# Kernel optimization log

Hardware: AMD Instinct MI355X
Metric: run time of the kernel (lower is better)

## Reference

```python
import jax, jax.numpy as jnp
import numpy as np

NG, NPG = 16384, 8            # graphs, nodes per graph
N = NG * NPG                   # total nodes
EPS = 1e-5                     # BatchNorm eps
SLOPE = 0.01                   # leaky_relu negative slope
DIMS = [6, 16, 16, 32, 64, 128]


def _gcn(x, src, dst, w_e, W, b):
    # PyG GCNConv with edge weights and implicit self-loops (weight 1):
    # h = x W; out = D^-1/2 (A + I) D^-1/2 h + b, deg from dst incl. self-loop
    h = x @ W
    deg = jnp.zeros((N,), h.dtype).at[dst].add(w_e) + 1.0
    dis = jax.lax.rsqrt(deg)
    norm = dis[src] * w_e * dis[dst]                      # [E]
    out = jnp.zeros_like(h).at[dst].add(norm[:, None] * h[src])
    out = out + h * (dis * dis)[:, None]                  # self-loop term deg^-1 * h
    return out + b


def _bn(x, g, be):
    # training-mode BatchNorm1d over nodes (biased variance)
    m = x.mean(0)
    v = ((x - m) ** 2).mean(0)
    return g * (x - m) * jax.lax.rsqrt(v + EPS) + be


def _lrelu(x):
    return jnp.where(x >= 0, x, SLOPE * x)


def setup_inputs() -> dict:
    key = jax.random.key(0)
    ks = jax.random.split(key, 16)
    # fully-connected directed edges within each 8-node graph (no self-loops)
    s, d = np.meshgrid(np.arange(NPG), np.arange(NPG), indexing='ij')
    m = s != d
    s, d = s[m], d[m]                                     # 56 per graph
    offs = (np.arange(NG) * NPG)[:, None]
    src = (offs + s[None, :]).ravel()
    dst = (offs + d[None, :]).ravel()
    E = src.size
    inp = {
        'x': jax.random.normal(ks[0], (N, DIMS[0]), jnp.float32),
        'edge_index': jnp.asarray(np.stack([src, dst]), dtype=jnp.int32),
        'edge_attr': jax.random.uniform(ks[1], (E,), jnp.float32),
        'batch': jnp.asarray(np.repeat(np.arange(NG), NPG), dtype=jnp.int32),
    }
    for i in range(5):
        inp[f'w{i+1}'] = jax.random.normal(ks[2 + i], (DIMS[i], DIMS[i + 1]), jnp.float32) * (1.0 / np.sqrt(DIMS[i]).astype(np.float32))
        inp[f'b{i+1}'] = jnp.zeros((DIMS[i + 1],), jnp.float32)
        inp[f'g{i+1}'] = jnp.ones((DIMS[i + 1],), jnp.float32)
        inp[f'be{i+1}'] = jnp.zeros((DIMS[i + 1],), jnp.float32)
    inp['fc1_w'] = jax.random.normal(ks[7], (128, 30), jnp.float32) * 0.1
    inp['fc1_b'] = jnp.zeros((30,), jnp.float32)
    inp['fc2_w'] = jax.random.normal(ks[8], (30, 20), jnp.float32) * 0.1
    inp['fc2_b'] = jnp.zeros((20,), jnp.float32)
    inp['out_w'] = jax.random.normal(ks[9], (20, 1), jnp.float32) * 0.1
    inp['out_b'] = jnp.zeros((1,), jnp.float32)
    return inp


def reference(x, edge_index, edge_attr, batch,
              w1, b1, g1, be1, w2, b2, g2, be2, w3, b3, g3, be3,
              w4, b4, g4, be4, w5, b5, g5, be5,
              fc1_w, fc1_b, fc2_w, fc2_b, out_w, out_b):
    src, dst = edge_index[0], edge_index[1]
    layers = [(w1, b1, g1, be1), (w2, b2, g2, be2), (w3, b3, g3, be3),
              (w4, b4, g4, be4), (w5, b5, g5, be5)]
    h = x
    for (W, b, g, be) in layers:
        h = _lrelu(_bn(_gcn(h, src, dst, edge_attr, W, b), g, be))
    # global mean pool: each graph has exactly NPG nodes
    pooled = jax.ops.segment_sum(h, batch, num_segments=NG) / NPG
    z = _lrelu(pooled @ fc1_w + fc1_b)
    z = _lrelu(z @ fc2_w + fc2_b)      # dropout is identity in eval mode
    return z @ out_w + out_b           # [NG, 1]
```

## Files before the change

kernel.cpp:

```cpp
#include <hip/hip_runtime.h>

#define NN 131072
#define NBLK 256
#define THREADS 512
#define NODES_B 512
#define GRAPHS_B 64
constexpr float BN_EPS = 1e-5f;
constexpr float NSLOPE = 0.01f;

typedef unsigned short ushortT;
typedef unsigned long long u64;
typedef short v8s __attribute__((ext_vector_type(8)));
typedef float v4f __attribute__((ext_vector_type(4)));

__device__ __forceinline__ float lrelu(float x) { return x >= 0.0f ? x : NSLOPE * x; }
__device__ __forceinline__ ushortT f2bf(float f) {
    unsigned int u = __float_as_uint(f);
    u += 0x7fffu + ((u >> 16) & 1u);
    return (ushortT)(u >> 16);
}

__device__ __forceinline__ u64 enc_stat(float t) {
    long long v = (long long)llrintf(t * 65536.0f) + (1LL << 41);
    return (1ULL << 52) + (u64)v;
}
__device__ __forceinline__ float dec_stat(u64 u) {
    long long v = (long long)(u & ((1ULL << 52) - 1)) - ((long long)NBLK << 41);
    return (float)((double)v * (1.0 / 65536.0));
}

__global__ void zero_ws_kernel(u64* __restrict__ p) {
    for (int i = threadIdx.x; i < 4096; i += 1024) p[i] = 0ULL;
}

struct Params {
    const float *x, *ea;
    const float *w1,*b1,*g1,*be1, *w2,*b2,*g2,*be2, *w3,*b3,*g3,*be3;
    const float *w4,*b4,*g4,*be4, *w5,*b5,*g5,*be5;
    const float *fc1w,*fc1b,*fc2w,*fc2b,*ow,*ob;
    u64* stats;
    float* outp;
};

template<int DIN>
__device__ __forceinline__ void agg_shfl(const float* xr, float* Y, const float* coef,
                                         int lane, int d) {
    #pragma unroll
    for (int k = 0; k < DIN; k++) Y[k] = coef[0] * xr[k];
    #pragma unroll
    for (int r = 1; r < 8; r++) {
        int srcLane = (lane & ~7) | ((d + r) & 7);
        float cr = coef[r];
        #pragma unroll
        for (int k = 0; k < DIN; k++)
            Y[k] = fmaf(cr, __shfl(xr[k], srcLane), Y[k]);
    }
}

template<int DIN, int DOUT>
__device__ __forceinline__ void gemm_lane(const float* Y, const float* Wl,
                                          const float* bias, float* acc) {
    #pragma unroll
    for (int j = 0; j < DOUT; j++) acc[j] = bias[j];
    #pragma unroll
    for (int k = 0; k < DIN; k++) {
        float yk = Y[k];
        #pragma unroll
        for (int j = 0; j < DOUT; j++)
            acc[j] = fmaf(yk, Wl[k * DOUT + j], acc[j]);
    }
}

template<int DOUT>
__device__ __forceinline__ void stats_from_hbuf(const float* hbuf, float* red,
                                                u64* statsL, int tid) {
    __syncthreads();
    constexpr int SEG = THREADS / DOUT;
    int c = tid % DOUT, seg = tid / DOUT;
    float s = 0.f, q = 0.f;
    #pragma unroll 4
    for (int i = 0; i < DOUT; i++) {
        float v = hbuf[(seg * DOUT + i) * 33 + c];
        s += v; q = fmaf(v, v, q);
    }
    red[seg * 2 * DOUT + c] = s;
    red[seg * 2 * DOUT + DOUT + c] = q;
    __syncthreads();
    if (tid < 2 * DOUT) {
        float t = 0.f;
        #pragma unroll
        for (int sg = 0; sg < SEG; sg++) t += red[sg * 2 * DOUT + tid];
        __hip_atomic_fetch_add(&statsL[tid * 8], enc_stat(t),
                               __ATOMIC_RELAXED, __HIP_MEMORY_SCOPE_AGENT);
    }
}

template<int DIN>
__device__ __forceinline__ void bn_params(const u64* statsL, const float* g,
                                          const float* be, float* scS, float* shS, int tid) {
    __syncthreads();
    if (tid < DIN) {
        u64 us, uq;
        int guard = 0;
        do {
            us = __hip_atomic_load(&statsL[tid * 8], __ATOMIC_RELAXED, __HIP_MEMORY_SCOPE_AGENT);
        } while ((us >> 52) < (u64)NBLK && ++guard < (1 << 26));
        guard = 0;
        do {
            uq = __hip_atomic_load(&statsL[(DIN + tid) * 8], __ATOMIC_RELAXED, __HIP_MEMORY_SCOPE_AGENT);
        } while ((uq >> 52) < (u64)NBLK && ++guard < (1 << 26));
        float s = dec_stat(us), q = dec_stat(uq);
        float mean = s * (1.0f / NN);
        float var = fmaf(-mean, mean, q * (1.0f / NN));
        float scl = g[tid] * rsqrtf(var + BN_EPS);
        scS[tid] = scl;
        shS[tid] = fmaf(-mean, scl, be[tid]);
    }
    __syncthreads();
}

__device__ __forceinline__ v8s ld_v8(const ushortT* p) {
    union { v8s v; uint2 u[2]; } t;
    t.u[0] = *(const uint2*)p;
    t.u[1] = *(const uint2*)(p + 4);
    return t.v;
}

#define SMEM_TOTAL 153472

__global__ __launch_bounds__(THREADS, 2) void fused_kernel(Params P)
{
    __shared__ __align__(16) char smem[SMEM_TOTAL];
    float*   hbuf   = (float*)smem;
    ushortT* Y4b    = (ushortT*)smem;
    ushortT* X5T    = (ushortT*)smem;
    float*   pooled = (float*)smem;
    float*   WesS   = (float*)(smem + 67584);
    float*   disS   = (float*)(smem + 81920);
    float*   AcS    = (float*)(smem + 83968);
    ushortT* X4T    = (ushortT*)(smem + 67584);
    ushortT* Y5b    = (ushortT*)(smem + 67584);
    float*   z1s    = (float*)(smem + 67584);
    float*   z2s    = (float*)(smem + 75776);
    float*   W123   = (float*)(smem + 137216);
    ushortT* W4t    = (ushortT*)(smem + 140672);
    float*   red    = (float*)(smem + 145280);
    float*   scS    = red;
    float*   shS    = red + 128;

    const int tid  = threadIdx.x;
    const int bid  = blockIdx.x;
    const int lane = tid & 63;
    const int w    = tid >> 6;
    const int m16  = lane & 15;
    const int quad = lane >> 4;
    const int d    = tid & 7;
    const int gloc = tid >> 3;

    const int g0 = bid * GRAPHS_B;
    for (int e = tid; e < GRAPHS_B * 56; e += THREADS) WesS[e] = P.ea[(size_t)g0 * 56 + e];
    if (tid < 96)  W123[tid] = P.w1[tid];
    if (tid < 256) W123[96 + tid] = P.w2[tid];
    W123[352 + tid] = P.w3[tid];
    for (int e = tid; e < 2048; e += THREADS) {
        int c = e >> 5, k = e & 31;
        W4t[c * 36 + k] = f2bf(P.w4[(size_t)k * 64 + c]);
    }
    __syncthreads();

    {
        float deg = 1.0f;
        #pragma unroll
        for (int s = 0; s < 8; s++)
            if (s != d) deg += WesS[gloc * 56 + s * 7 + (d > s ? d - 1 : d)];
        disS[tid] = rsqrtf(deg);
    }
    __syncthreads();

    float coef[8];
    {
        float dis = disS[tid];
        coef[0] = dis * dis;
        #pragma unroll
        for (int r = 1; r < 8; r++) {
            int s = (d + r) & 7;
            float we = WesS[gloc * 56 + s * 7 + (d > s ? d - 1 : d)];
            coef[r] = dis * we * disS[(tid & ~7) | s];
        }
    }
    for (int e = tid; e < GRAPHS_B * 64; e += THREADS) {
        int g = e >> 6, s = (e >> 3) & 7, dd = e & 7;
        float v;
        if (s == dd) { float t = disS[g * 8 + dd]; v = t * t; }
        else v = disS[g * 8 + s] * WesS[g * 56 + s * 7 + (dd > s ? dd - 1 : dd)] * disS[g * 8 + dd];
        AcS[g * 68 + s * 8 + dd] = v;
    }
    __syncthreads();

    v8s AcM[4];
    #pragma unroll
    for (int Gl = 0; Gl < 4; Gl++) {
        int G = 4 * w + Gl;
        int koct = 2 * (G & 1) + (m16 >> 3);
        int gA = 2 * G + (m16 >> 3);
        ushortT tmp[8];
        #pragma unroll
        for (int j = 0; j < 8; j++)
            tmp[j] = (quad == koct) ? f2bf(AcS[gA * 68 + j * 8 + (m16 & 7)]) : (ushortT)0;
        AcM[Gl] = *(v8s*)tmp;
    }
    v8s W5f[8][2];
    #pragma unroll
    for (int ct = 0; ct < 8; ct++)
        #pragma unroll
        for (int kh = 0; kh < 2; kh++) {
            ushortT tmp[8];
            #pragma unroll
            for (int j = 0; j < 8; j++)
                tmp[j] = f2bf(P.w5[(size_t)(kh * 32 + quad * 8 + j) * 128 + ct * 16 + m16]);
            W5f[ct][kh] = *(v8s*)tmp;
        }

    const int gnode = bid * NODES_B + tid;
    float xr[16];
    {
        const float2* px = (const float2*)(P.x + (size_t)gnode * 6);
        float2 a = px[0], b = px[1], c = px[2];
        xr[0]=a.x; xr[1]=a.y; xr[2]=b.x; xr[3]=b.y; xr[4]=c.x; xr[5]=c.y;
    }
    {
        float Y[6], acc[16];
        agg_shfl<6>(xr, Y, coef, lane, d);
        gemm_lane<6,16>(Y, W123, P.b1, acc);
        #pragma unroll
        for (int j = 0; j < 16; j++) hbuf[tid * 33 + j] = acc[j];
    }
    stats_from_hbuf<16>(hbuf, red, P.stats + 0, tid);
    bn_params<16>(P.stats + 0, P.g1, P.be1, scS, shS, tid);

    {
        #pragma unroll
        for (int k = 0; k < 16; k++)
            xr[k] = lrelu(fmaf(scS[k], hbuf[tid * 33 + k], shS[k]));
        float Y[16], acc[16];
        agg_shfl<16>(xr, Y, coef, lane, d);
        gemm_lane<16,16>(Y, W123 + 96, P.b2, acc);
        #pragma unroll
        for (int j = 0; j < 16; j++) hbuf[tid * 33 + j] = acc[j];
    }
    stats_from_hbuf<16>(hbuf, red, P.stats + 32 * 8, tid);
    bn_params<16>(P.stats + 32 * 8, P.g2, P.be2, scS, shS, tid);

    {
        #pragma unroll
        for (int k = 0; k < 16; k++)
            xr[k] = lrelu(fmaf(scS[k], hbuf[tid * 33 + k], shS[k]));
        float Y[16], acc[32];
        agg_shfl<16>(xr, Y, coef, lane, d);
        gemm_lane<16,32>(Y, W123 + 352, P.b3, acc);
        #pragma unroll
        for (int j = 0; j < 32; j++) hbuf[tid * 33 + j] = acc[j];
    }
    stats_from_hbuf<32>(hbuf, red, P.stats + 64 * 8, tid);
    bn_params<32>(P.stats + 64 * 8, P.g3, P.be3, scS, shS, tid);

    #pragma unroll
    for (int it = 0; it < 8; it++) {
        int item = tid + it * THREADS;
        int c = item & 31, nq = item >> 5;
        float sc = scS[c], sh = shS[c];
        ushortT pk[4];
        #pragma unroll
        for (int i = 0; i < 4; i++)
            pk[i] = f2bf(lrelu(fmaf(sc, hbuf[(nq * 4 + i) * 33 + c], sh)));
        *(uint2*)&X4T[c * 520 + nq * 4] = *(uint2*)pk;
    }
    __syncthreads();

    {
        v8s Bf[2][2];
        #pragma unroll
        for (int Jl = 0; Jl < 2; Jl++) {
            int J = 2 * w + Jl;
            #pragma unroll
            for (int ct = 0; ct < 2; ct++)
                Bf[Jl][ct] = ld_v8(&X4T[(ct * 16 + m16) * 520 + 32 * J + quad * 8]);
        }
        #pragma unroll
        for (int Gl = 0; Gl < 4; Gl++) {
            int G = 4 * w + Gl;
            #pragma unroll
            for (int ct = 0; ct < 2; ct++) {
                v4f a = (v4f){0.f, 0.f, 0.f, 0.f};
                a = __builtin_amdgcn_mfma_f32_16x16x32_bf16(AcM[Gl], Bf[Gl >> 1][ct], a, 0, 0, 0);
                int ch = ct * 16 + m16;
                #pragma unroll
                for (int r = 0; r < 4; r++)
                    Y4b[(G * 16 + quad * 4 + r) * 36 + ch] = f2bf(a[r]);
            }
        }
    }
    __syncthreads();

    float b4r[4];
    #pragma unroll
    for (int ct = 0; ct < 4; ct++) b4r[ct] = P.b4[ct * 16 + m16];
    v4f acc4[4][4];
    {
        v8s W4fr[4];
        #pragma unroll
        for (int ct = 0; ct < 4; ct++)
            W4fr[ct] = ld_v8(&W4t[(ct * 16 + m16) * 36 + quad * 8]);
        #pragma unroll
        for (int rt = 0; rt < 4; rt++) {
            v8s Af = ld_v8(&Y4b[(w * 64 + rt * 16 + m16) * 36 + quad * 8]);
            #pragma unroll
            for (int ct = 0; ct < 4; ct++) {
                v4f a = (v4f){0.f, 0.f, 0.f, 0.f};
                a = __builtin_amdgcn_mfma_f32_16x16x32_bf16(Af, W4fr[ct], a, 0, 0, 0);
                #pragma unroll
                for (int r = 0; r < 4; r++) a[r] += b4r[ct];
                acc4[rt][ct] = a;
            }
        }
    }
    {
        float ps[4], pq[4];
        #pragma unroll
        for (int ct = 0; ct < 4; ct++) { ps[ct] = 0.f; pq[ct] = 0.f; }
        #pragma unroll
        for (int rt = 0; rt < 4; rt++)
            #pragma unroll
            for (int ct = 0; ct < 4; ct++)
                #pragma unroll
                for (int r = 0; r < 4; r++) {
                    float v = acc4[rt][ct][r];
                    ps[ct] += v; pq[ct] = fmaf(v, v, pq[ct]);
                }
        __syncthreads();
        #pragma unroll
        for (int ct = 0; ct < 4; ct++) {
            float s = ps[ct], q = pq[ct];
            s += __shfl_xor(s, 16); s += __shfl_xor(s, 32);
            q += __shfl_xor(q, 16); q += __shfl_xor(q, 32);
            if (lane < 16) {
                red[w * 256 + ct * 16 + lane] = s;
                red[w * 256 + 64 + ct * 16 + lane] = q;
            }
        }
        __syncthreads();
        if (tid < 128) {
            float t = 0.f;
            #pragma unroll
            for (int ww = 0; ww < 8; ww++) t += red[ww * 256 + tid];
            __hip_atomic_fetch_add(&P.stats[(128 + tid) * 8], enc_stat(t),
                                   __ATOMIC_RELAXED, __HIP_MEMORY_SCOPE_AGENT);
        }
    }
    bn_params<64>(P.stats + 128 * 8, P.g4, P.be4, scS, shS, tid);

    #pragma unroll
    for (int rt = 0; rt < 4; rt++) {
        int nd0 = w * 64 + rt * 16 + quad * 4;
        #pragma unroll
        for (int ct = 0; ct < 4; ct++) {
            int c = ct * 16 + m16;
            float sc = scS[c], sh = shS[c];
            ushortT pk[4];
            #pragma unroll
            for (int r = 0; r < 4; r++)
                pk[r] = f2bf(lrelu(fmaf(sc, acc4[rt][ct][r], sh)));
            *(uint2*)&X5T[c * 520 + nd0] = *(uint2*)pk;
        }
    }
    __syncthreads();

    {
        v8s Bf[2][4];
        #pragma unroll
        for (int Jl = 0; Jl < 2; Jl++) {
            int J = 2 * w + Jl;
            #pragma unroll
            for (int ct = 0; ct < 4; ct++)
                Bf[Jl][ct] = ld_v8(&X5T[(ct * 16 + m16) * 520 + 32 * J + quad * 8]);
        }
        #pragma unroll
        for (int Gl = 0; Gl < 4; Gl++) {
            int G = 4 * w + Gl;
            #pragma unroll
            for (int ct = 0; ct < 4; ct++) {
                v4f a = (v4f){0.f, 0.f, 0.f, 0.f};
                a = __builtin_amdgcn_mfma_f32_16x16x32_bf16(AcM[Gl], Bf[Gl >> 1][ct], a, 0, 0, 0);
                int ch = ct * 16 + m16;
                #pragma unroll
                for (int r = 0; r < 4; r++)
                    Y5b[(G * 16 + quad * 4 + r) * 68 + ch] = f2bf(a[r]);
            }
        }
    }
    __syncthreads();

    float b5r[8];
    #pragma unroll
    for (int ct = 0; ct < 8; ct++) b5r[ct] = P.b5[ct * 16 + m16];
    v4f acc5[4][8];
    #pragma unroll
    for (int rt = 0; rt < 4; rt++) {
        v8s Af0 = ld_v8(&Y5b[(w * 64 + rt * 16 + m16) * 68 + quad * 8]);
        v8s Af1 = ld_v8(&Y5b[(w * 64 + rt * 16 + m16) * 68 + 32 + quad * 8]);
        #pragma unroll
        for (int ct = 0; ct < 8; ct++) {
            v4f a = (v4f){0.f, 0.f, 0.f, 0.f};
            a = __builtin_amdgcn_mfma_f32_16x16x32_bf16(Af0, W5f[ct][0], a, 0, 0, 0);
            a = __builtin_amdgcn_mfma_f32_16x16x32_bf16(Af1, W5f[ct][1], a, 0, 0, 0);
            #pragma unroll
            for (int r = 0; r < 4; r++) a[r] += b5r[ct];
            acc5[rt][ct] = a;
        }
    }
    {
        float ps[8], pq[8];
        #pragma unroll
        for (int ct = 0; ct < 8; ct++) { ps[ct] = 0.f; pq[ct] = 0.f; }
        #pragma unroll
        for (int rt = 0; rt < 4; rt++)
            #pragma unroll
            for (int ct = 0; ct < 8; ct++)
                #pragma unroll
                for (int r = 0; r < 4; r++) {
                    float v = acc5[rt][ct][r];
                    ps[ct] += v; pq[ct] = fmaf(v, v, pq[ct]);
                }
        __syncthreads();
        #pragma unroll
        for (int ct = 0; ct < 8; ct++) {
            float s = ps[ct], q = pq[ct];
            s += __shfl_xor(s, 16); s += __shfl_xor(s, 32);
            q += __shfl_xor(q, 16); q += __shfl_xor(q, 32);
            if (lane < 16) {
                red[w * 256 + ct * 16 + lane] = s;
                red[w * 256 + 128 + ct * 16 + lane] = q;
            }
        }
        __syncthreads();
        if (tid < 256) {
            float t = 0.f;
            #pragma unroll
            for (int ww = 0; ww < 8; ww++) t += red[ww * 256 + tid];
            __hip_atomic_fetch_add(&P.stats[(256 + tid) * 8], enc_stat(t),
                                   __ATOMIC_RELAXED, __HIP_MEMORY_SCOPE_AGENT);
        }
    }
    bn_params<128>(P.stats + 256 * 8, P.g5, P.be5, scS, shS, tid);

    #pragma unroll
    for (int rt = 0; rt < 4; rt++) {
        int gA = 8 * w + 2 * rt + (quad >> 1);
        #pragma unroll
        for (int ct = 0; ct < 8; ct++) {
            int c = ct * 16 + m16;
            float sc = scS[c], sh = shS[c];
            float p = 0.f;
            #pragma unroll
            for (int r = 0; r < 4; r++)
                p += lrelu(fmaf(sc, acc5[rt][ct][r], sh));
            p += __shfl_xor(p, 16);
            if ((quad & 1) == 0) pooled[gA * 132 + c] = p * 0.125f;
        }
    }
    __syncthreads();

    const int t32 = tid & 31, gg = tid >> 5;
    for (int pass = 0; pass < 4; pass++) {
        int g = gg + pass * 16;
        if (t32 < 30) {
            float a = P.fc1b[t32];
            for (int k = 0; k < 128; k++) a = fmaf(pooled[g * 132 + k], P.fc1w[k * 30 + t32], a);
            z1s[g * 32 + t32] = lrelu(a);
        }
        __syncthreads();
        if (t32 < 20) {
            float a = P.fc2b[t32];
            #pragma unroll
            for (int k = 0; k < 30; k++) a = fmaf(z1s[g * 32 + k], P.fc2w[k * 20 + t32], a);
            z2s[g * 32 + t32] = lrelu(a);
        }
        __syncthreads();
        if (t32 == 0) {
            float a = P.ob[0];
            #pragma unroll
            for (int k = 0; k < 20; k++) a = fmaf(z2s[g * 32 + k], P.ow[k], a);
            P.outp[bid * GRAPHS_B + g] = a;
        }
        __syncthreads();
    }
}

extern "C" void kernel_launch(void* const* d_in, const int* in_sizes, int n_in,
                              void* d_out, int out_size, void* d_ws, size_t ws_size,
                              hipStream_t stream)
{
    (void)in_sizes; (void)n_in; (void)out_size; (void)ws_size;
    u64* stats = (u64*)d_ws;

    Params hp;
    hp.x   = (const float*)d_in[0];
    hp.ea  = (const float*)d_in[2];
    hp.w1  = (const float*)d_in[4];  hp.b1  = (const float*)d_in[5];
    hp.g1  = (const float*)d_in[6];  hp.be1 = (const float*)d_in[7];
    hp.w2  = (const float*)d_in[8];  hp.b2  = (const float*)d_in[9];
    hp.g2  = (const float*)d_in[10]; hp.be2 = (const float*)d_in[11];
    hp.w3  = (const float*)d_in[12]; hp.b3  = (const float*)d_in[13];
    hp.g3  = (const float*)d_in[14]; hp.be3 = (const float*)d_in[15];
    hp.w4  = (const float*)d_in[16]; hp.b4  = (const float*)d_in[17];
    hp.g4  = (const float*)d_in[18]; hp.be4 = (const float*)d_in[19];
    hp.w5  = (const float*)d_in[20]; hp.b5  = (const float*)d_in[21];
    hp.g5  = (const float*)d_in[22]; hp.be5 = (const float*)d_in[23];
    hp.fc1w = (const float*)d_in[24]; hp.fc1b = (const float*)d_in[25];
    hp.fc2w = (const float*)d_in[26]; hp.fc2b = (const float*)d_in[27];
    hp.ow   = (const float*)d_in[28]; hp.ob   = (const float*)d_in[29];
    hp.stats = stats;
    hp.outp  = (float*)d_out;

    zero_ws_kernel<<<1, 1024, 0, stream>>>(stats);
    fused_kernel<<<NBLK, THREADS, 0, stream>>>(hp);
}
```

Before: 228.2 us.

## Compute MLP head with bf16 MFMA and hoist layer-1 work before setup

The final FC1/FC2 head was a scalar loop of four passes with many block barriers. It is replaced by bf16 MFMA tiles: one 16x16x32 MFMA chain per wave for FC1 and a single MFMA for FC2, with zero-padded intermediate buffers. Layer-1 aggregation, GEMM and stats are also moved earlier, before the A-matrix and W4 staging, so global stats atomics can overlap that setup work. This cuts barriers and scalar FMAs but lowers the head's precision to bf16 and uses more shared-memory layout changes.

```diff
diff --git a/kernel.cpp b/kernel.cpp
--- a/kernel.cpp
+++ b/kernel.cpp
@@ -140,8 +140,8 @@
     float*   AcS    = (float*)(smem + 83968);
     ushortT* X4T    = (ushortT*)(smem + 67584);
     ushortT* Y5b    = (ushortT*)(smem + 67584);
-    float*   z1s    = (float*)(smem + 67584);
-    float*   z2s    = (float*)(smem + 75776);
+    ushortT* z1b    = (ushortT*)(smem + 67584);
+    float*   z2f    = (float*)(smem + 72704);
     float*   W123   = (float*)(smem + 137216);
     ushortT* W4t    = (ushortT*)(smem + 140672);
     float*   red    = (float*)(smem + 145280);
@@ -162,10 +162,6 @@
     if (tid < 96)  W123[tid] = P.w1[tid];
     if (tid < 256) W123[96 + tid] = P.w2[tid];
     W123[352 + tid] = P.w3[tid];
-    for (int e = tid; e < 2048; e += THREADS) {
-        int c = e >> 5, k = e & 31;
-        W4t[c * 36 + k] = f2bf(P.w4[(size_t)k * 64 + c]);
-    }
     __syncthreads();
 
     {
@@ -188,6 +184,23 @@
             coef[r] = dis * we * disS[(tid & ~7) | s];
         }
     }
+
+    const int gnode = bid * NODES_B + tid;
+    float xr[16];
+    {
+        const float2* px = (const float2*)(P.x + (size_t)gnode * 6);
+        float2 a = px[0], b = px[1], c = px[2];
+        xr[0]=a.x; xr[1]=a.y; xr[2]=b.x; xr[3]=b.y; xr[4]=c.x; xr[5]=c.y;
+    }
+    {
+        float Y[6], acc[16];
+        agg_shfl<6>(xr, Y, coef, lane, d);
+        gemm_lane<6,16>(Y, W123, P.b1, acc);
+        #pragma unroll
+        for (int j = 0; j < 16; j++) hbuf[tid * 33 + j] = acc[j];
+    }
+    stats_from_hbuf<16>(hbuf, red, P.stats + 0, tid);
+
     for (int e = tid; e < GRAPHS_B * 64; e += THREADS) {
         int g = e >> 6, s = (e >> 3) & 7, dd = e & 7;
         float v;
@@ -195,6 +208,10 @@
         else v = disS[g * 8 + s] * WesS[g * 56 + s * 7 + (dd > s ? dd - 1 : dd)] * disS[g * 8 + dd];
         AcS[g * 68 + s * 8 + dd] = v;
     }
+    for (int e = tid; e < 2048; e += THREADS) {
+        int c = e >> 5, k = e & 31;
+        W4t[c * 36 + k] = f2bf(P.w4[(size_t)k * 64 + c]);
+    }
     __syncthreads();
 
     v8s AcM[4];
@@ -221,21 +238,6 @@
             W5f[ct][kh] = *(v8s*)tmp;
         }
 
-    const int gnode = bid * NODES_B + tid;
-    float xr[16];
-    {
-        const float2* px = (const float2*)(P.x + (size_t)gnode * 6);
-        float2 a = px[0], b = px[1], c = px[2];
-        xr[0]=a.x; xr[1]=a.y; xr[2]=b.x; xr[3]=b.y; xr[4]=c.x; xr[5]=c.y;
-    }
-    {
-        float Y[6], acc[16];
-        agg_shfl<6>(xr, Y, coef, lane, d);
-        gemm_lane<6,16>(Y, W123, P.b1, acc);
-        #pragma unroll
-        for (int j = 0; j < 16; j++) hbuf[tid * 33 + j] = acc[j];
-    }
-    stats_from_hbuf<16>(hbuf, red, P.stats + 0, tid);
     bn_params<16>(P.stats + 0, P.g1, P.be1, scS, shS, tid);
 
     {
@@ -468,31 +470,68 @@
             if ((quad & 1) == 0) pooled[gA * 132 + c] = p * 0.125f;
         }
     }
-    __syncthreads();
-
-    const int t32 = tid & 31, gg = tid >> 5;
-    for (int pass = 0; pass < 4; pass++) {
-        int g = gg + pass * 16;
-        if (t32 < 30) {
-            float a = P.fc1b[t32];
-            for (int k = 0; k < 128; k++) a = fmaf(pooled[g * 132 + k], P.fc1w[k * 30 + t32], a);
-            z1s[g * 32 + t32] = lrelu(a);
-        }
-        __syncthreads();
-        if (t32 < 20) {
-            float a = P.fc2b[t32];
-            #pragma unroll
-            for (int k = 0; k < 30; k++) a = fmaf(z1s[g * 32 + k], P.fc2w[k * 20 + t32], a);
-            z2s[g * 32 + t32] = lrelu(a);
-        }
-        __syncthreads();
-        if (t32 == 0) {
-            float a = P.ob[0];
-            #pragma unroll
-            for (int k = 0; k < 20; k++) a = fmaf(z2s[g * 32 + k], P.ow[k], a);
-            P.outp[bid * GRAPHS_B + g] = a;
-        }
-        __syncthreads();
+    for (int e = tid; e < 640; e += THREADS) {
+        int g = e / 10, c = 30 + e % 10;
+        z1b[g * 40 + c] = (ushortT)0;
+    }
+    __syncthreads();
+
+    {
+        int rt = w & 3, ct = w >> 2;
+        int tcol = ct * 16 + m16;
+        v4f a = (v4f){0.f, 0.f, 0.f, 0.f};
+        #pragma unroll
+        for (int kh = 0; kh < 4; kh++) {
+            const float* pr = &pooled[(rt * 16 + m16) * 132 + kh * 32 + quad * 8];
+            float4 p0 = *(const float4*)pr;
+            float4 p1 = *(const float4*)(pr + 4);
+            ushortT at[8] = { f2bf(p0.x), f2bf(p0.y), f2bf(p0.z), f2bf(p0.w),
+                              f2bf(p1.x), f2bf(p1.y), f2bf(p1.z), f2bf(p1.w) };
+            ushortT bt[8];
+            #pragma unroll
+            for (int j = 0; j < 8; j++)
+                bt[j] = (tcol < 30) ? f2bf(P.fc1w[(size_t)(kh * 32 + quad * 8 + j) * 30 + tcol]) : (ushortT)0;
+            a = __builtin_amdgcn_mfma_f32_16x16x32_bf16(*(v8s*)at, *(v8s*)bt, a, 0, 0, 0);
+        }
+        if (tcol < 30) {
+            float bb = P.fc1b[tcol];
+            #pragma unroll
+            for (int r = 0; r < 4; r++) {
+                int g = rt * 16 + quad * 4 + r;
+                z1b[g * 40 + tcol] = f2bf(lrelu(a[r] + bb));
+            }
+        }
+    }
+    __syncthreads();
+
+    {
+        int rt = w & 3, ct = w >> 2;
+        int tcol = ct * 16 + m16;
+        v8s af = ld_v8(&z1b[(rt * 16 + m16) * 40 + quad * 8]);
+        ushortT bt[8];
+        #pragma unroll
+        for (int j = 0; j < 8; j++) {
+            int k = quad * 8 + j;
+            bt[j] = (k < 30 && tcol < 20) ? f2bf(P.fc2w[k * 20 + tcol]) : (ushortT)0;
+        }
+        v4f a = (v4f){0.f, 0.f, 0.f, 0.f};
+        a = __builtin_amdgcn_mfma_f32_16x16x32_bf16(af, *(v8s*)bt, a, 0, 0, 0);
+        if (tcol < 20) {
+            float bb = P.fc2b[tcol];
+            #pragma unroll
+            for (int r = 0; r < 4; r++) {
+                int g = rt * 16 + quad * 4 + r;
+                z2f[g * 21 + tcol] = lrelu(a[r] + bb);
+            }
+        }
+    }
+    __syncthreads();
+
+    if (tid < 64) {
+        float a = P.ob[0];
+        #pragma unroll
+        for (int k = 0; k < 20; k++) a = fmaf(z2f[tid * 21 + k], P.ow[k], a);
+        P.outp[bid * GRAPHS_B + tid] = a;
     }
 }
 
```

Result: faster. 217.2 us (-4.8%).
